# Kernel tuning notes

Hardware: AMD Instinct MI355X
Metric: run time of the kernel (lower is better)

Reference implementation:

```python
import jax, jax.numpy as jnp
import numpy as np

N_NODES = 20000
DEG = 32
N_EDGES = N_NODES * DEG
NUM_USERS = 100000
D = 128


def setup_inputs() -> dict:
    key = jax.random.key(0)
    ks = jax.random.split(key, 10)
    nodes = jax.random.randint(ks[0], (N_NODES,), 0, NUM_USERS)
    neigh_idx = jax.random.randint(ks[1], (N_EDGES,), 0, NUM_USERS)
    # fixed-degree flattening of the ragged to_neighs lists: every node has DEG neighbors
    seg_ids = jnp.repeat(jnp.arange(N_NODES), DEG)
    u2e = jax.random.normal(ks[2], (NUM_USERS, D), dtype=jnp.float32)
    W1 = jax.random.normal(ks[3], (2 * D, D), dtype=jnp.float32) * 0.05
    b1 = jax.random.normal(ks[4], (D,), dtype=jnp.float32) * 0.05
    W2 = jax.random.normal(ks[5], (D, D), dtype=jnp.float32) * 0.05
    b2 = jax.random.normal(ks[6], (D,), dtype=jnp.float32) * 0.05
    w3 = jax.random.normal(ks[7], (D, 1), dtype=jnp.float32) * 0.05
    b3 = jax.random.normal(ks[8], (1,), dtype=jnp.float32) * 0.05
    return {"nodes": nodes, "neigh_idx": neigh_idx, "seg_ids": seg_ids,
            "u2e": u2e, "W1": W1, "b1": b1, "W2": W2, "b2": b2, "w3": w3, "b3": b3}


def reference(nodes, neigh_idx, seg_ids, u2e, W1, b1, W2, b2, w3, b3):
    n = nodes.shape[0]
    e_u = u2e[neigh_idx]                 # [E, D] neighbor embeddings
    u_rep = u2e[nodes][seg_ids]          # [E, D] center-node embedding repeated per neighbor
    x = jnp.concatenate([e_u, u_rep], axis=1)        # [E, 2D]
    h = jax.nn.relu(x @ W1 + b1)                      # [E, D]
    h = jax.nn.relu(h @ W2 + b2)                      # [E, D]
    s = (h @ w3 + b3)[:, 0]                           # [E] attention logits
    # segment softmax over each node's neighbor set
    smax = jax.ops.segment_max(s, seg_ids, num_segments=n)
    e = jnp.exp(s - smax[seg_ids])
    denom = jax.ops.segment_sum(e, seg_ids, num_segments=n)
    att = e / denom[seg_ids]                          # [E]
    # attention-weighted neighbor sum (e_u^T @ att per node)
    out = jax.ops.segment_sum(att[:, None] * e_u, seg_ids, num_segments=n)  # [N, D]
    return out
```

## Files before the change

kernel.cpp:

```cpp
#include <hip/hip_runtime.h>
#include <hip/hip_bf16.h>

#define DD 128
#define DEG 32

typedef __attribute__((ext_vector_type(8))) short short8;
typedef __attribute__((ext_vector_type(8))) _Float16 half8;
typedef __attribute__((ext_vector_type(4))) float f32x4;

__device__ __forceinline__ ushort f2bs(float x) {
    __hip_bfloat16 h = __float2bfloat16(x);
    return *reinterpret_cast<ushort*>(&h);
}
__device__ __forceinline__ unsigned pack2(float a, float b) {
    return (unsigned)f2bs(a) | ((unsigned)f2bs(b) << 16);
}
__device__ __forceinline__ unsigned relu_add_pack(unsigned p, unsigned q) {
    float a0 = __uint_as_float(p << 16)        + __uint_as_float(q << 16);
    float a1 = __uint_as_float(p & 0xffff0000u) + __uint_as_float(q & 0xffff0000u);
    return pack2(fmaxf(a0, 0.f), fmaxf(a1, 0.f));
}

__global__ __launch_bounds__(256) void k_prep(
    const float* __restrict__ W1, const float* __restrict__ W2,
    uint4* __restrict__ w1img, uint4* __restrict__ w2t)
{
    int t = blockIdx.x * 256 + threadIdx.x;
    if (t < 4096) {
        int l = t & 63, f = t >> 6, k4 = f & 3, nt = f >> 2;
        int n = nt * 16 + (l & 15), kb = k4 * 32 + ((l >> 4) & 3) * 8;
        float v[8];
        #pragma unroll
        for (int i = 0; i < 8; ++i) {
            int k = kb + i;
            v[i] = (n < DD) ? W1[k * DD + n] : W1[(DD + k) * DD + (n - DD)];
        }
        uint4 r;
        r.x = pack2(v[0], v[1]); r.y = pack2(v[2], v[3]);
        r.z = pack2(v[4], v[5]); r.w = pack2(v[6], v[7]);
        w1img[t] = r;
    } else if (t < 6144) {
        int q = t - 4096;
        int l = q & 63, f = q >> 6, k4 = f & 3, mt = f >> 2;
        int ch = mt * 16 + (l & 15), kb = k4 * 32 + ((l >> 4) & 3) * 8;
        float v[8];
        #pragma unroll
        for (int i = 0; i < 8; ++i) v[i] = W2[(kb + i) * DD + ch];
        uint4 r;
        r.x = pack2(v[0], v[1]); r.y = pack2(v[2], v[3]);
        r.z = pack2(v[4], v[5]); r.w = pack2(v[6], v[7]);
        w2t[q] = r;
    }
}

__global__ __launch_bounds__(256) void k_pq(
    const float* __restrict__ u2e, const float* __restrict__ b1,
    const short8* __restrict__ w1img, ushort* __restrict__ Pb,
    ushort* __restrict__ Qb, _Float16* __restrict__ e16, int U)
{
    const int t = threadIdx.x;
    const int w = t >> 6, l = t & 63;
    const int base = blockIdx.x * 128;

    short8 a[2][4];
    #pragma unroll
    for (int mt = 0; mt < 2; ++mt) {
        int user = base + w * 32 + mt * 16 + (l & 15);
        int ruser = min(user, U - 1);
        const float* rp = u2e + (size_t)ruser * DD + ((l >> 4) << 3);
        #pragma unroll
        for (int k4 = 0; k4 < 4; ++k4) {
            float4 v0 = *reinterpret_cast<const float4*>(rp + k4 * 32);
            float4 v1 = *reinterpret_cast<const float4*>(rp + k4 * 32 + 4);
            uint4 r;
            r.x = pack2(v0.x, v0.y); r.y = pack2(v0.z, v0.w);
            r.z = pack2(v1.x, v1.y); r.w = pack2(v1.z, v1.w);
            a[mt][k4] = *reinterpret_cast<short8*>(&r);
            if (user < U) {
                half8 hv;
                hv[0] = (_Float16)v0.x; hv[1] = (_Float16)v0.y;
                hv[2] = (_Float16)v0.z; hv[3] = (_Float16)v0.w;
                hv[4] = (_Float16)v1.x; hv[5] = (_Float16)v1.y;
                hv[6] = (_Float16)v1.z; hv[7] = (_Float16)v1.w;
                *reinterpret_cast<half8*>(
                    &e16[(size_t)user * DD + k4 * 32 + ((l >> 4) << 3)]) = hv;
            }
        }
    }

    const int chq = (l >> 4) << 2;
    #pragma unroll 2
    for (int mt = 0; mt < 8; ++mt) {
        short8 wf[4];
        #pragma unroll
        for (int k4 = 0; k4 < 4; ++k4) wf[k4] = w1img[(mt * 4 + k4) * 64 + l];
        #pragma unroll
        for (int ntu = 0; ntu < 2; ++ntu) {
            f32x4 acc = {0.f, 0.f, 0.f, 0.f};
            #pragma unroll
            for (int k4 = 0; k4 < 4; ++k4)
                acc = __builtin_amdgcn_mfma_f32_16x16x32_bf16(wf[k4], a[ntu][k4], acc, 0, 0, 0);
            int user = base + w * 32 + ntu * 16 + (l & 15);
            if (user < U) {
                uint2 pk;
                pk.x = pack2(acc[0], acc[1]); pk.y = pack2(acc[2], acc[3]);
                *reinterpret_cast<uint2*>(&Pb[(size_t)user * DD + mt * 16 + chq]) = pk;
            }
        }
    }
    #pragma unroll 2
    for (int mt = 8; mt < 16; ++mt) {
        short8 wf[4];
        #pragma unroll
        for (int k4 = 0; k4 < 4; ++k4) wf[k4] = w1img[(mt * 4 + k4) * 64 + l];
        float4 b1v = *reinterpret_cast<const float4*>(&b1[(mt - 8) * 16 + chq]);
        #pragma unroll
        for (int ntu = 0; ntu < 2; ++ntu) {
            f32x4 acc = {0.f, 0.f, 0.f, 0.f};
            #pragma unroll
            for (int k4 = 0; k4 < 4; ++k4)
                acc = __builtin_amdgcn_mfma_f32_16x16x32_bf16(wf[k4], a[ntu][k4], acc, 0, 0, 0);
            int user = base + w * 32 + ntu * 16 + (l & 15);
            if (user < U) {
                uint2 pk;
                pk.x = pack2(acc[0] + b1v.x, acc[1] + b1v.y);
                pk.y = pack2(acc[2] + b1v.z, acc[3] + b1v.w);
                *reinterpret_cast<uint2*>(&Qb[(size_t)user * DD + (mt - 8) * 16 + chq]) = pk;
            }
        }
    }
}

__global__ __launch_bounds__(256) void k_node(
    const int* __restrict__ nodes, const int* __restrict__ neigh,
    const _Float16* __restrict__ e16, const ushort* __restrict__ Pb,
    const ushort* __restrict__ Qb, const short8* __restrict__ w2t,
    const float* __restrict__ b2, const float* __restrict__ w3,
    float4* __restrict__ out4, int n)
{
    const int t = threadIdx.x;
    const int w = t >> 6, l = t & 63;
    const int node = blockIdx.x * 4 + w;
    if (node >= n) return;

    const int lane16 = l & 15;
    const int koff = (l >> 4) << 3;
    const int jg = l >> 4;

    const int u    = nodes[node];
    const int idx0 = neigh[node * DEG + lane16];
    const int idx1 = neigh[node * DEG + 16 + lane16];

    uint4 qv[4];
    #pragma unroll
    for (int k4 = 0; k4 < 4; ++k4)
        qv[k4] = *reinterpret_cast<const uint4*>(&Qb[(size_t)u * DD + k4 * 32 + koff]);
    uint4 pv0[4], pv1[4];
    #pragma unroll
    for (int k4 = 0; k4 < 4; ++k4)
        pv0[k4] = *reinterpret_cast<const uint4*>(&Pb[(size_t)idx0 * DD + k4 * 32 + koff]);
    #pragma unroll
    for (int k4 = 0; k4 < 4; ++k4)
        pv1[k4] = *reinterpret_cast<const uint4*>(&Pb[(size_t)idx1 * DD + k4 * 32 + koff]);

    short8 hb0[4], hb1[4];
    #pragma unroll
    for (int k4 = 0; k4 < 4; ++k4) {
        uint4 r;
        r.x = relu_add_pack(pv0[k4].x, qv[k4].x);
        r.y = relu_add_pack(pv0[k4].y, qv[k4].y);
        r.z = relu_add_pack(pv0[k4].z, qv[k4].z);
        r.w = relu_add_pack(pv0[k4].w, qv[k4].w);
        hb0[k4] = *reinterpret_cast<short8*>(&r);
        uint4 s;
        s.x = relu_add_pack(pv1[k4].x, qv[k4].x);
        s.y = relu_add_pack(pv1[k4].y, qv[k4].y);
        s.z = relu_add_pack(pv1[k4].z, qv[k4].z);
        s.w = relu_add_pack(pv1[k4].w, qv[k4].w);
        hb1[k4] = *reinterpret_cast<short8*>(&s);
    }

    float pl0 = 0.f, pl1 = 0.f;
    #pragma unroll
    for (int mt = 0; mt < 8; ++mt) {
        short8 wf[4];
        #pragma unroll
        for (int k4 = 0; k4 < 4; ++k4) wf[k4] = w2t[(mt * 4 + k4) * 64 + l];
        float4 b2v = *reinterpret_cast<const float4*>(&b2[mt * 16 + (l >> 4) * 4]);
        float4 w3v = *reinterpret_cast<const float4*>(&w3[mt * 16 + (l >> 4) * 4]);
        f32x4 a0 = {0.f, 0.f, 0.f, 0.f}, a1 = {0.f, 0.f, 0.f, 0.f};
        #pragma unroll
        for (int k4 = 0; k4 < 4; ++k4)
            a0 = __builtin_amdgcn_mfma_f32_16x16x32_bf16(wf[k4], hb0[k4], a0, 0, 0, 0);
        #pragma unroll
        for (int k4 = 0; k4 < 4; ++k4)
            a1 = __builtin_amdgcn_mfma_f32_16x16x32_bf16(wf[k4], hb1[k4], a1, 0, 0, 0);
        pl0 += fmaxf(a0[0] + b2v.x, 0.f) * w3v.x + fmaxf(a0[1] + b2v.y, 0.f) * w3v.y
             + fmaxf(a0[2] + b2v.z, 0.f) * w3v.z + fmaxf(a0[3] + b2v.w, 0.f) * w3v.w;
        pl1 += fmaxf(a1[0] + b2v.x, 0.f) * w3v.x + fmaxf(a1[1] + b2v.y, 0.f) * w3v.y
             + fmaxf(a1[2] + b2v.z, 0.f) * w3v.z + fmaxf(a1[3] + b2v.w, 0.f) * w3v.w;
    }
    pl0 += __shfl_xor(pl0, 16); pl0 += __shfl_xor(pl0, 32);
    pl1 += __shfl_xor(pl1, 16); pl1 += __shfl_xor(pl1, 32);

    float mx = fmaxf(pl0, pl1);
    #pragma unroll
    for (int mask = 1; mask <= 8; mask <<= 1) mx = fmaxf(mx, __shfl_xor(mx, mask));
    float e0 = __expf(pl0 - mx), e1 = __expf(pl1 - mx);
    float sm = e0 + e1;
    #pragma unroll
    for (int mask = 1; mask <= 8; mask <<= 1) sm += __shfl_xor(sm, mask);
    float inv = __frcp_rn(sm);
    float att0 = e0 * inv, att1 = e1 * inv;

    int   nbj[8];
    half8 pre[8];
    #pragma unroll
    for (int j = 0; j < 8; ++j)
        nbj[j] = neigh[node * DEG + jg * 8 + j];
    #pragma unroll
    for (int j = 0; j < 8; ++j)
        pre[j] = *reinterpret_cast<const half8*>(&e16[(size_t)nbj[j] * DD + lane16 * 8]);

    float o[8] = {0.f, 0.f, 0.f, 0.f, 0.f, 0.f, 0.f, 0.f};
    #pragma unroll
    for (int j = 0; j < 8; ++j) {
        int e = jg * 8 + j;
        float alo = __shfl(att0, e & 15);
        float ahi = __shfl(att1, e & 15);
        float a = (jg < 2) ? alo : ahi;
        #pragma unroll
        for (int i = 0; i < 8; ++i) o[i] = fmaf(a, (float)pre[j][i], o[i]);
    }
    #pragma unroll
    for (int i = 0; i < 8; ++i) {
        o[i] += __shfl_xor(o[i], 16);
        o[i] += __shfl_xor(o[i], 32);
    }
    if (l < 16) {
        float4 r0 = make_float4(o[0], o[1], o[2], o[3]);
        float4 r1 = make_float4(o[4], o[5], o[6], o[7]);
        out4[(size_t)node * 32 + lane16 * 2]     = r0;
        out4[(size_t)node * 32 + lane16 * 2 + 1] = r1;
    }
}

extern "C" void kernel_launch(void* const* d_in, const int* in_sizes, int n_in,
                              void* d_out, int out_size, void* d_ws, size_t ws_size,
                              hipStream_t stream)
{
    const int*   nodes = (const int*)  d_in[0];
    const int*   neigh = (const int*)  d_in[1];
    const float* u2e   = (const float*)d_in[3];
    const float* W1    = (const float*)d_in[4];
    const float* b1    = (const float*)d_in[5];
    const float* W2    = (const float*)d_in[6];
    const float* b2    = (const float*)d_in[7];
    const float* w3    = (const float*)d_in[8];

    const int n = in_sizes[0];
    const int U = in_sizes[3] / DD;

    uint4*     w1img = (uint4*)d_ws;
    uint4*     w2t   = w1img + 4096;
    ushort*    Pb    = (ushort*)(w2t + 2048);
    ushort*    Qb    = Pb + (size_t)U * DD;
    _Float16*  e16   = (_Float16*)(Qb + (size_t)U * DD);

    k_prep<<<24, 256, 0, stream>>>(W1, W2, w1img, w2t);
    k_pq<<<(U + 127) / 128, 256, 0, stream>>>(u2e, b1, (const short8*)w1img,
                                              Pb, Qb, e16, U);
    k_node<<<(n + 3) / 4, 256, 0, stream>>>(nodes, neigh, e16,
                                            Pb, Qb,
                                            (const short8*)w2t, b2, w3,
                                            (float4*)d_out, n);
}
```

Before: 110.1 us.

## Compute neighbor layer-1 per edge in node kernel instead of precomputing P for all users

Drops the per-user P precomputation: the first GEMM on neighbor embeddings now runs per edge inside the node kernel, with both weight images staged in LDS. The Q term is computed only for the center nodes rather than all users, and a plain fp16 cast kernel replaces the bf16/fp16 dual writes. Everything moves from bf16 to fp16 MFMA. Layer-1 outputs are reshuffled across lanes into the B-operand layout, and the final weighted sum reuses the neighbor embeddings already in registers instead of gathering them again. This trades extra MFMA work (32 edges per node versus 100k users) plus shuffle overhead for much less gather and write traffic.

```diff
diff --git a/kernel.cpp b/kernel.cpp
--- a/kernel.cpp
+++ b/kernel.cpp
@@ -4,21 +4,19 @@
 #define DD 128
 #define DEG 32
 
-typedef __attribute__((ext_vector_type(8))) short short8;
 typedef __attribute__((ext_vector_type(8))) _Float16 half8;
 typedef __attribute__((ext_vector_type(4))) float f32x4;
 
-__device__ __forceinline__ ushort f2bs(float x) {
-    __hip_bfloat16 h = __float2bfloat16(x);
-    return *reinterpret_cast<ushort*>(&h);
-}
-__device__ __forceinline__ unsigned pack2(float a, float b) {
-    return (unsigned)f2bs(a) | ((unsigned)f2bs(b) << 16);
-}
-__device__ __forceinline__ unsigned relu_add_pack(unsigned p, unsigned q) {
-    float a0 = __uint_as_float(p << 16)        + __uint_as_float(q << 16);
-    float a1 = __uint_as_float(p & 0xffff0000u) + __uint_as_float(q & 0xffff0000u);
-    return pack2(fmaxf(a0, 0.f), fmaxf(a1, 0.f));
+__device__ __forceinline__ unsigned pkh(float a, float b) {
+    _Float16 ha = (_Float16)a, hb = (_Float16)b;
+    return (unsigned)__builtin_bit_cast(unsigned short, ha)
+         | ((unsigned)__builtin_bit_cast(unsigned short, hb) << 16);
+}
+__device__ __forceinline__ float h2f_lo(unsigned u) {
+    return (float)__builtin_bit_cast(_Float16, (unsigned short)(u & 0xffff));
+}
+__device__ __forceinline__ float h2f_hi(unsigned u) {
+    return (float)__builtin_bit_cast(_Float16, (unsigned short)(u >> 16));
 }
 
 __global__ __launch_bounds__(256) void k_prep(
@@ -36,8 +34,8 @@
             v[i] = (n < DD) ? W1[k * DD + n] : W1[(DD + k) * DD + (n - DD)];
         }
         uint4 r;
-        r.x = pack2(v[0], v[1]); r.y = pack2(v[2], v[3]);
-        r.z = pack2(v[4], v[5]); r.w = pack2(v[6], v[7]);
+        r.x = pkh(v[0], v[1]); r.y = pkh(v[2], v[3]);
+        r.z = pkh(v[4], v[5]); r.w = pkh(v[6], v[7]);
         w1img[t] = r;
     } else if (t < 6144) {
         int q = t - 4096;
@@ -47,154 +45,167 @@
         #pragma unroll
         for (int i = 0; i < 8; ++i) v[i] = W2[(kb + i) * DD + ch];
         uint4 r;
-        r.x = pack2(v[0], v[1]); r.y = pack2(v[2], v[3]);
-        r.z = pack2(v[4], v[5]); r.w = pack2(v[6], v[7]);
+        r.x = pkh(v[0], v[1]); r.y = pkh(v[2], v[3]);
+        r.z = pkh(v[4], v[5]); r.w = pkh(v[6], v[7]);
         w2t[q] = r;
     }
 }
 
-__global__ __launch_bounds__(256) void k_pq(
-    const float* __restrict__ u2e, const float* __restrict__ b1,
-    const short8* __restrict__ w1img, ushort* __restrict__ Pb,
-    ushort* __restrict__ Qb, _Float16* __restrict__ e16, int U)
-{
-    const int t = threadIdx.x;
-    const int w = t >> 6, l = t & 63;
+__global__ __launch_bounds__(256) void k_cast(
+    const float4* __restrict__ u2e4, uint4* __restrict__ ub16v, int total8)
+{
+    int i = blockIdx.x * 256 + threadIdx.x;
+    if (i >= total8) return;
+    float4 v0 = u2e4[(size_t)i * 2], v1 = u2e4[(size_t)i * 2 + 1];
+    uint4 r;
+    r.x = pkh(v0.x, v0.y); r.y = pkh(v0.z, v0.w);
+    r.z = pkh(v1.x, v1.y); r.w = pkh(v1.z, v1.w);
+    ub16v[i] = r;
+}
+
+__global__ __launch_bounds__(256) void k_qn(
+    const int* __restrict__ nodes, const float* __restrict__ u2e,
+    const uint4* __restrict__ w1img, const float* __restrict__ b1,
+    unsigned short* __restrict__ Qnh, int n)
+{
+    const int t = threadIdx.x, w = t >> 6, l = t & 63;
     const int base = blockIdx.x * 128;
 
-    short8 a[2][4];
-    #pragma unroll
-    for (int mt = 0; mt < 2; ++mt) {
-        int user = base + w * 32 + mt * 16 + (l & 15);
-        int ruser = min(user, U - 1);
-        const float* rp = u2e + (size_t)ruser * DD + ((l >> 4) << 3);
+    half8 a[2][4];
+    #pragma unroll
+    for (int nt = 0; nt < 2; ++nt) {
+        int row = min(base + w * 32 + nt * 16 + (l & 15), n - 1);
+        int user = nodes[row];
+        const float* rp = u2e + (size_t)user * DD + ((l >> 4) << 3);
         #pragma unroll
         for (int k4 = 0; k4 < 4; ++k4) {
             float4 v0 = *reinterpret_cast<const float4*>(rp + k4 * 32);
             float4 v1 = *reinterpret_cast<const float4*>(rp + k4 * 32 + 4);
             uint4 r;
-            r.x = pack2(v0.x, v0.y); r.y = pack2(v0.z, v0.w);
-            r.z = pack2(v1.x, v1.y); r.w = pack2(v1.z, v1.w);
-            a[mt][k4] = *reinterpret_cast<short8*>(&r);
-            if (user < U) {
-                half8 hv;
-                hv[0] = (_Float16)v0.x; hv[1] = (_Float16)v0.y;
-                hv[2] = (_Float16)v0.z; hv[3] = (_Float16)v0.w;
-                hv[4] = (_Float16)v1.x; hv[5] = (_Float16)v1.y;
-                hv[6] = (_Float16)v1.z; hv[7] = (_Float16)v1.w;
-                *reinterpret_cast<half8*>(
-                    &e16[(size_t)user * DD + k4 * 32 + ((l >> 4) << 3)]) = hv;
-            }
-        }
-    }
-
+            r.x = pkh(v0.x, v0.y); r.y = pkh(v0.z, v0.w);
+            r.z = pkh(v1.x, v1.y); r.w = pkh(v1.z, v1.w);
+            a[nt][k4] = __builtin_bit_cast(half8, r);
+        }
+    }
     const int chq = (l >> 4) << 2;
-    #pragma unroll 2
+    #pragma unroll
     for (int mt = 0; mt < 8; ++mt) {
-        short8 wf[4];
-        #pragma unroll
-        for (int k4 = 0; k4 < 4; ++k4) wf[k4] = w1img[(mt * 4 + k4) * 64 + l];
-        #pragma unroll
-        for (int ntu = 0; ntu < 2; ++ntu) {
+        half8 wf[4];
+        #pragma unroll
+        for (int k4 = 0; k4 < 4; ++k4)
+            wf[k4] = __builtin_bit_cast(half8, w1img[((8 + mt) * 4 + k4) * 64 + l]);
+        float4 b1v = *reinterpret_cast<const float4*>(&b1[mt * 16 + chq]);
+        #pragma unroll
+        for (int nt = 0; nt < 2; ++nt) {
             f32x4 acc = {0.f, 0.f, 0.f, 0.f};
             #pragma unroll
             for (int k4 = 0; k4 < 4; ++k4)
-                acc = __builtin_amdgcn_mfma_f32_16x16x32_bf16(wf[k4], a[ntu][k4], acc, 0, 0, 0);
-            int user = base + w * 32 + ntu * 16 + (l & 15);
-            if (user < U) {
+                acc = __builtin_amdgcn_mfma_f32_16x16x32_f16(wf[k4], a[nt][k4], acc, 0, 0, 0);
+            int row = base + w * 32 + nt * 16 + (l & 15);
+            if (row < n) {
                 uint2 pk;
-                pk.x = pack2(acc[0], acc[1]); pk.y = pack2(acc[2], acc[3]);
-                *reinterpret_cast<uint2*>(&Pb[(size_t)user * DD + mt * 16 + chq]) = pk;
+                pk.x = pkh(acc[0] + b1v.x, acc[1] + b1v.y);
+                pk.y = pkh(acc[2] + b1v.z, acc[3] + b1v.w);
+                *reinterpret_cast<uint2*>(&Qnh[(size_t)row * DD + mt * 16 + chq]) = pk;
             }
         }
     }
-    #pragma unroll 2
-    for (int mt = 8; mt < 16; ++mt) {
-        short8 wf[4];
-        #pragma unroll
-        for (int k4 = 0; k4 < 4; ++k4) wf[k4] = w1img[(mt * 4 + k4) * 64 + l];
-        float4 b1v = *reinterpret_cast<const float4*>(&b1[(mt - 8) * 16 + chq]);
-        #pragma unroll
-        for (int ntu = 0; ntu < 2; ++ntu) {
-            f32x4 acc = {0.f, 0.f, 0.f, 0.f};
-            #pragma unroll
-            for (int k4 = 0; k4 < 4; ++k4)
-                acc = __builtin_amdgcn_mfma_f32_16x16x32_bf16(wf[k4], a[ntu][k4], acc, 0, 0, 0);
-            int user = base + w * 32 + ntu * 16 + (l & 15);
-            if (user < U) {
-                uint2 pk;
-                pk.x = pack2(acc[0] + b1v.x, acc[1] + b1v.y);
-                pk.y = pack2(acc[2] + b1v.z, acc[3] + b1v.w);
-                *reinterpret_cast<uint2*>(&Qb[(size_t)user * DD + (mt - 8) * 16 + chq]) = pk;
-            }
-        }
-    }
-}
-
-__global__ __launch_bounds__(256) void k_node(
-    const int* __restrict__ nodes, const int* __restrict__ neigh,
-    const _Float16* __restrict__ e16, const ushort* __restrict__ Pb,
-    const ushort* __restrict__ Qb, const short8* __restrict__ w2t,
-    const float* __restrict__ b2, const float* __restrict__ w3,
-    float4* __restrict__ out4, int n)
-{
-    const int t = threadIdx.x;
-    const int w = t >> 6, l = t & 63;
-    const int node = blockIdx.x * 4 + w;
-    if (node >= n) return;
-
-    const int lane16 = l & 15;
-    const int koff = (l >> 4) << 3;
-    const int jg = l >> 4;
-
-    const int u    = nodes[node];
-    const int idx0 = neigh[node * DEG + lane16];
-    const int idx1 = neigh[node * DEG + 16 + lane16];
-
-    uint4 qv[4];
+}
+
+__global__ __launch_bounds__(512, 4) void k_node(
+    const int* __restrict__ neigh, const _Float16* __restrict__ ub16,
+    const unsigned short* __restrict__ Qnh, const uint4* __restrict__ w1img,
+    const uint4* __restrict__ w2t, const float* __restrict__ b2,
+    const float* __restrict__ w3, float4* __restrict__ out4, int n)
+{
+    __shared__ uint4 s_img[4096];
+
+    const int t = threadIdx.x, w = t >> 6, l = t & 63;
+    const int node = min(blockIdx.x * 8 + w, n - 1);
+    const int g = l >> 4, c = l & 15;
+
+    #pragma unroll
+    for (int i = 0; i < 4; ++i) s_img[i * 512 + t] = w1img[i * 512 + t];
+    #pragma unroll
+    for (int i = 0; i < 4; ++i) s_img[2048 + i * 512 + t] = w2t[i * 512 + t];
+
+    const int idx0 = neigh[node * DEG + c];
+    const int idx1 = neigh[node * DEG + 16 + c];
+    const int koff = g * 8;
+    half8 ub0[4], ub1[4];
     #pragma unroll
     for (int k4 = 0; k4 < 4; ++k4)
-        qv[k4] = *reinterpret_cast<const uint4*>(&Qb[(size_t)u * DD + k4 * 32 + koff]);
-    uint4 pv0[4], pv1[4];
+        ub0[k4] = *reinterpret_cast<const half8*>(&ub16[(size_t)idx0 * DD + k4 * 32 + koff]);
     #pragma unroll
     for (int k4 = 0; k4 < 4; ++k4)
-        pv0[k4] = *reinterpret_cast<const uint4*>(&Pb[(size_t)idx0 * DD + k4 * 32 + koff]);
-    #pragma unroll
-    for (int k4 = 0; k4 < 4; ++k4)
-        pv1[k4] = *reinterpret_cast<const uint4*>(&Pb[(size_t)idx1 * DD + k4 * 32 + koff]);
-
-    short8 hb0[4], hb1[4];
+        ub1[k4] = *reinterpret_cast<const half8*>(&ub16[(size_t)idx1 * DD + k4 * 32 + koff]);
+    uint2 qnh[8];
+    #pragma unroll
+    for (int mt = 0; mt < 8; ++mt)
+        qnh[mt] = *reinterpret_cast<const uint2*>(&Qnh[(size_t)node * DD + mt * 16 + g * 4]);
+
+    __syncthreads();
+
+    uint2 hp0[8], hp1[8];
+    #pragma unroll
+    for (int mt = 0; mt < 8; ++mt) {
+        half8 wf[4];
+        #pragma unroll
+        for (int k4 = 0; k4 < 4; ++k4)
+            wf[k4] = __builtin_bit_cast(half8, s_img[(mt * 4 + k4) * 64 + l]);
+        f32x4 a0 = {0.f, 0.f, 0.f, 0.f}, a1 = {0.f, 0.f, 0.f, 0.f};
+        #pragma unroll
+        for (int k4 = 0; k4 < 4; ++k4)
+            a0 = __builtin_amdgcn_mfma_f32_16x16x32_f16(wf[k4], ub0[k4], a0, 0, 0, 0);
+        #pragma unroll
+        for (int k4 = 0; k4 < 4; ++k4)
+            a1 = __builtin_amdgcn_mfma_f32_16x16x32_f16(wf[k4], ub1[k4], a1, 0, 0, 0);
+        float q0 = h2f_lo(qnh[mt].x), q1 = h2f_hi(qnh[mt].x);
+        float q2 = h2f_lo(qnh[mt].y), q3 = h2f_hi(qnh[mt].y);
+        hp0[mt].x = pkh(fmaxf(a0[0] + q0, 0.f), fmaxf(a0[1] + q1, 0.f));
+        hp0[mt].y = pkh(fmaxf(a0[2] + q2, 0.f), fmaxf(a0[3] + q3, 0.f));
+        hp1[mt].x = pkh(fmaxf(a1[0] + q0, 0.f), fmaxf(a1[1] + q1, 0.f));
+        hp1[mt].y = pkh(fmaxf(a1[2] + q2, 0.f), fmaxf(a1[3] + q3, 0.f));
+    }
+
+    const int srcA = ((g & 1) << 5) + c;
+    const int hiSel = g >> 1;
+    half8 hb0[4], hb1[4];
     #pragma unroll
     for (int k4 = 0; k4 < 4; ++k4) {
-        uint4 r;
-        r.x = relu_add_pack(pv0[k4].x, qv[k4].x);
-        r.y = relu_add_pack(pv0[k4].y, qv[k4].y);
-        r.z = relu_add_pack(pv0[k4].z, qv[k4].z);
-        r.w = relu_add_pack(pv0[k4].w, qv[k4].w);
-        hb0[k4] = *reinterpret_cast<short8*>(&r);
-        uint4 s;
-        s.x = relu_add_pack(pv1[k4].x, qv[k4].x);
-        s.y = relu_add_pack(pv1[k4].y, qv[k4].y);
-        s.z = relu_add_pack(pv1[k4].z, qv[k4].z);
-        s.w = relu_add_pack(pv1[k4].w, qv[k4].w);
-        hb1[k4] = *reinterpret_cast<short8*>(&s);
+        unsigned d[4], e[4];
+        #pragma unroll
+        for (int j = 0; j < 4; ++j) {
+            int src = srcA + ((j >> 1) << 4);
+            unsigned vE = (unsigned)__shfl((int)((j & 1) ? hp0[2 * k4].y : hp0[2 * k4].x), src);
+            unsigned vO = (unsigned)__shfl((int)((j & 1) ? hp0[2 * k4 + 1].y : hp0[2 * k4 + 1].x), src);
+            d[j] = hiSel ? vO : vE;
+            unsigned uE = (unsigned)__shfl((int)((j & 1) ? hp1[2 * k4].y : hp1[2 * k4].x), src);
+            unsigned uO = (unsigned)__shfl((int)((j & 1) ? hp1[2 * k4 + 1].y : hp1[2 * k4 + 1].x), src);
+            e[j] = hiSel ? uO : uE;
+        }
+        uint4 du = {d[0], d[1], d[2], d[3]};
+        uint4 eu = {e[0], e[1], e[2], e[3]};
+        hb0[k4] = __builtin_bit_cast(half8, du);
+        hb1[k4] = __builtin_bit_cast(half8, eu);
     }
 
     float pl0 = 0.f, pl1 = 0.f;
     #pragma unroll
     for (int mt = 0; mt < 8; ++mt) {
-        short8 wf[4];
-        #pragma unroll
-        for (int k4 = 0; k4 < 4; ++k4) wf[k4] = w2t[(mt * 4 + k4) * 64 + l];
-        float4 b2v = *reinterpret_cast<const float4*>(&b2[mt * 16 + (l >> 4) * 4]);
-        float4 w3v = *reinterpret_cast<const float4*>(&w3[mt * 16 + (l >> 4) * 4]);
+        half8 wf[4];
+        #pragma unroll
+        for (int k4 = 0; k4 < 4; ++k4)
+            wf[k4] = __builtin_bit_cast(half8, s_img[2048 + (mt * 4 + k4) * 64 + l]);
+        float4 b2v = *reinterpret_cast<const float4*>(&b2[mt * 16 + g * 4]);
+        float4 w3v = *reinterpret_cast<const float4*>(&w3[mt * 16 + g * 4]);
         f32x4 a0 = {0.f, 0.f, 0.f, 0.f}, a1 = {0.f, 0.f, 0.f, 0.f};
         #pragma unroll
         for (int k4 = 0; k4 < 4; ++k4)
-            a0 = __builtin_amdgcn_mfma_f32_16x16x32_bf16(wf[k4], hb0[k4], a0, 0, 0, 0);
-        #pragma unroll
-        for (int k4 = 0; k4 < 4; ++k4)
-            a1 = __builtin_amdgcn_mfma_f32_16x16x32_bf16(wf[k4], hb1[k4], a1, 0, 0, 0);
+            a0 = __builtin_amdgcn_mfma_f32_16x16x32_f16(wf[k4], hb0[k4], a0, 0, 0, 0);
+        #pragma unroll
+        for (int k4 = 0; k4 < 4; ++k4)
+            a1 = __builtin_amdgcn_mfma_f32_16x16x32_f16(wf[k4], hb1[k4], a1, 0, 0, 0);
         pl0 += fmaxf(a0[0] + b2v.x, 0.f) * w3v.x + fmaxf(a0[1] + b2v.y, 0.f) * w3v.y
              + fmaxf(a0[2] + b2v.z, 0.f) * w3v.z + fmaxf(a0[3] + b2v.w, 0.f) * w3v.w;
         pl1 += fmaxf(a1[0] + b2v.x, 0.f) * w3v.x + fmaxf(a1[1] + b2v.y, 0.f) * w3v.y
@@ -213,35 +224,28 @@
     float inv = __frcp_rn(sm);
     float att0 = e0 * inv, att1 = e1 * inv;
 
-    int   nbj[8];
-    half8 pre[8];
-    #pragma unroll
-    for (int j = 0; j < 8; ++j)
-        nbj[j] = neigh[node * DEG + jg * 8 + j];
-    #pragma unroll
-    for (int j = 0; j < 8; ++j)
-        pre[j] = *reinterpret_cast<const half8*>(&e16[(size_t)nbj[j] * DD + lane16 * 8]);
-
-    float o[8] = {0.f, 0.f, 0.f, 0.f, 0.f, 0.f, 0.f, 0.f};
-    #pragma unroll
-    for (int j = 0; j < 8; ++j) {
-        int e = jg * 8 + j;
-        float alo = __shfl(att0, e & 15);
-        float ahi = __shfl(att1, e & 15);
-        float a = (jg < 2) ? alo : ahi;
-        #pragma unroll
-        for (int i = 0; i < 8; ++i) o[i] = fmaf(a, (float)pre[j][i], o[i]);
-    }
-    #pragma unroll
-    for (int i = 0; i < 8; ++i) {
-        o[i] += __shfl_xor(o[i], 16);
-        o[i] += __shfl_xor(o[i], 32);
-    }
-    if (l < 16) {
-        float4 r0 = make_float4(o[0], o[1], o[2], o[3]);
-        float4 r1 = make_float4(o[4], o[5], o[6], o[7]);
-        out4[(size_t)node * 32 + lane16 * 2]     = r0;
-        out4[(size_t)node * 32 + lane16 * 2 + 1] = r1;
+    float o[4][8];
+    #pragma unroll
+    for (int k4 = 0; k4 < 4; ++k4)
+        #pragma unroll
+        for (int i = 0; i < 8; ++i)
+            o[k4][i] = att0 * (float)ub0[k4][i] + att1 * (float)ub1[k4][i];
+    #pragma unroll
+    for (int mask = 1; mask <= 8; mask <<= 1) {
+        #pragma unroll
+        for (int k4 = 0; k4 < 4; ++k4)
+            #pragma unroll
+            for (int i = 0; i < 8; ++i)
+                o[k4][i] += __shfl_xor(o[k4][i], mask);
+    }
+    if (c == 0) {
+        #pragma unroll
+        for (int k4 = 0; k4 < 4; ++k4) {
+            float4 r0 = make_float4(o[k4][0], o[k4][1], o[k4][2], o[k4][3]);
+            float4 r1 = make_float4(o[k4][4], o[k4][5], o[k4][6], o[k4][7]);
+            out4[(size_t)node * 32 + k4 * 8 + g * 2]     = r0;
+            out4[(size_t)node * 32 + k4 * 8 + g * 2 + 1] = r1;
+        }
     }
 }
 
@@ -261,17 +265,17 @@
     const int n = in_sizes[0];
     const int U = in_sizes[3] / DD;
 
-    uint4*     w1img = (uint4*)d_ws;
-    uint4*     w2t   = w1img + 4096;
-    ushort*    Pb    = (ushort*)(w2t + 2048);
-    ushort*    Qb    = Pb + (size_t)U * DD;
-    _Float16*  e16   = (_Float16*)(Qb + (size_t)U * DD);
+    uint4*          w1img = (uint4*)d_ws;
+    uint4*          w2t   = w1img + 4096;
+    _Float16*       ub16  = (_Float16*)(w2t + 2048);
+    unsigned short* Qnh   = (unsigned short*)(ub16 + (size_t)U * DD);
+
+    const int total8 = U * (DD / 8);
 
     k_prep<<<24, 256, 0, stream>>>(W1, W2, w1img, w2t);
-    k_pq<<<(U + 127) / 128, 256, 0, stream>>>(u2e, b1, (const short8*)w1img,
-                                              Pb, Qb, e16, U);
-    k_node<<<(n + 3) / 4, 256, 0, stream>>>(nodes, neigh, e16,
-                                            Pb, Qb,
-                                            (const short8*)w2t, b2, w3,
-                                            (float4*)d_out, n);
-}
+    k_cast<<<(total8 + 255) / 256, 256, 0, stream>>>(
+        (const float4*)u2e, (uint4*)ub16, total8);
+    k_qn<<<(n + 127) / 128, 256, 0, stream>>>(nodes, u2e, w1img, b1, Qnh, n);
+    k_node<<<(n + 7) / 8, 512, 0, stream>>>(neigh, ub16, Qnh, w1img, w2t,
+                                            b2, w3, (float4*)d_out, n);
+}
```

New measurement: 108.3 us. Within noise of the previous version (-1.6%).
